# Kernel tuning notes

Hardware: AMD Instinct MI355X
Metric: run time of the kernel (lower is better)

Reference implementation:

```python
import jax, jax.numpy as jnp
import numpy as np


def setup_inputs() -> dict:
    key = jax.random.key(0)
    ks = jax.random.split(key, 18)
    B, L, D, E, V = 64, 4096, 512, 256, 32000
    s = 0.05
    return {
        "featureGrid": jax.random.normal(ks[0], (B, L, D), jnp.float32),
        "y_prev": jax.random.uniform(ks[1], (B, V), jnp.float32),
        "out_prev": jax.random.normal(ks[2], (B, D), jnp.float32),
        "h_prev": jax.random.normal(ks[3], (B, D), jnp.float32),
        "c_prev": jax.random.normal(ks[4], (B, D), jnp.float32),
        "embedding": jax.random.normal(ks[5], (V, E), jnp.float32) * s,
        "W_f": jax.random.normal(ks[6], (D + E, D), jnp.float32) * s,
        "W_i": jax.random.normal(ks[7], (D + E, D), jnp.float32) * s,
        "W_g": jax.random.normal(ks[8], (D + E, D), jnp.float32) * s,
        "W_o": jax.random.normal(ks[9], (D + E, D), jnp.float32) * s,
        "b_f": jax.random.normal(ks[10], (D,), jnp.float32) * s,
        "b_i": jax.random.normal(ks[11], (D,), jnp.float32) * s,
        "b_g": jax.random.normal(ks[12], (D,), jnp.float32) * s,
        "b_o": jax.random.normal(ks[13], (D,), jnp.float32) * s,
        "W_e": jax.random.normal(ks[14], (D, D), jnp.float32) * s,
        "W_out": jax.random.normal(ks[15], (2 * D, D), jnp.float32) * s,
        "W_y": jax.random.normal(ks[16], (D, V), jnp.float32) * s,
    }


def reference(featureGrid, y_prev, out_prev, h_prev, c_prev, embedding,
              W_f, W_i, W_g, W_o, b_f, b_i, b_g, b_o, W_e, W_out, W_y):
    # free_run: previous output distribution -> argmax token -> embedding
    tok = jnp.argmax(y_prev, axis=-1)              # [B]
    emb = embedding[tok]                            # [B, E]
    x = jnp.concatenate([emb, out_prev], axis=-1)   # [B, E+D]
    f = jax.nn.sigmoid(x @ W_f + b_f)
    i = jax.nn.sigmoid(x @ W_i + b_i)
    g = jnp.tanh(x @ W_g + b_g)
    o = jax.nn.sigmoid(x @ W_o + b_o)
    c = c_prev * f + i * g                          # [B, D]
    h = jnp.tanh(c) * o                             # [B, D]
    b = h @ W_e                                     # [B, D]
    e = jnp.einsum('bld,bd->bl', featureGrid, b)    # attention scores [B, L]
    a = jax.nn.softmax(e, axis=-1)                  # [B, L]
    z = jnp.einsum('bl,bld->bd', a, featureGrid)    # context [B, D]
    hz = jnp.concatenate([h, z], axis=-1)           # [B, 2D]
    out = jnp.tanh(hz @ W_out)                      # [B, D]
    y = jax.nn.softmax(out @ W_y, axis=-1)          # [B, V]
    return (y, out, h, c)
```

## Files before the change

kernel.cpp:

```cpp
#include <hip/hip_runtime.h>
#include <math.h>

#define NB 64
#define NL 4096
#define ND 512
#define NE 256
#define NV 32000
#define NX 768
#define CHUNKS 32
#define RPC (NL / CHUNKS)
#define RPW (RPC / 4)
#define NV4 (NV / 4)

#define GK_KS 4
#define GK_KL 192
#define WE_KS 4
#define WE_KL 128
#define WO_KS 4
#define WO_KL 256

typedef float v4f __attribute__((ext_vector_type(4)));
__device__ __forceinline__ float4 ntload4(const float* p) {
    v4f v = __builtin_nontemporal_load((const v4f*)p);
    return make_float4(v[0], v[1], v[2], v[3]);
}

__global__ void k_argmax(const float* __restrict__ y_prev, int* __restrict__ tok) {
    int b = blockIdx.x, tid = threadIdx.x, lane = tid & 63, wave = tid >> 6;
    const float4* row = (const float4*)(y_prev + (size_t)b * NV);
    float best = -INFINITY; int bi = 0x7fffffff;
    for (int v4 = tid; v4 < NV4; v4 += 1024) {
        float4 x = row[v4];
        int base = v4 * 4;
        if (x.x > best) { best = x.x; bi = base; }
        if (x.y > best) { best = x.y; bi = base + 1; }
        if (x.z > best) { best = x.z; bi = base + 2; }
        if (x.w > best) { best = x.w; bi = base + 3; }
    }
    #pragma unroll
    for (int off = 32; off > 0; off >>= 1) {
        float ob = __shfl_xor(best, off, 64);
        int   oi = __shfl_xor(bi, off, 64);
        if (ob > best || (ob == best && oi < bi)) { best = ob; bi = oi; }
    }
    __shared__ float sv[16]; __shared__ int si[16];
    if (lane == 0) { sv[wave] = best; si[wave] = bi; }
    __syncthreads();
    if (tid == 0) {
        float bb = sv[0]; int ii = si[0];
        for (int w = 1; w < 16; ++w)
            if (sv[w] > bb || (sv[w] == bb && si[w] < ii)) { bb = sv[w]; ii = si[w]; }
        tok[b] = ii;
    }
}

__global__ void k_gates(const float* __restrict__ embedding, const float* __restrict__ out_prev,
                        const int* __restrict__ tok,
                        const float* __restrict__ W_f, const float* __restrict__ W_i,
                        const float* __restrict__ W_g, const float* __restrict__ W_o,
                        float* __restrict__ gp) {
    __shared__ float xs[16][GK_KL];
    int tid = threadIdx.x;
    int cc = blockIdx.x, bg = blockIdx.y, ks = blockIdx.z;
    int k0 = ks * GK_KL;
    for (int e = tid; e < 16 * GK_KL; e += 256) {
        int bi = e / GK_KL, kk = e - bi * GK_KL;
        int b = bg * 16 + bi, k = k0 + kk;
        xs[bi][kk] = (k < NE) ? embedding[(size_t)tok[b] * NE + k]
                              : out_prev[(size_t)b * ND + (k - NE)];
    }
    __syncthreads();
    int ct = tid & 63, bs = tid >> 6;
    int gate = cc >> 1;
    int d = (cc & 1) * 256 + ct * 4;
    const float* W = (gate == 0) ? W_f : (gate == 1) ? W_i : (gate == 2) ? W_g : W_o;
    const float4* Wp = (const float4*)(W + (size_t)k0 * ND + d);
    float acc[4][4] = {};
    #pragma unroll 4
    for (int kk = 0; kk < GK_KL; ++kk) {
        float4 w4 = Wp[kk * (ND / 4)];
        #pragma unroll
        for (int i = 0; i < 4; ++i) {
            float xv = xs[bs * 4 + i][kk];
            acc[i][0] += xv * w4.x; acc[i][1] += xv * w4.y;
            acc[i][2] += xv * w4.z; acc[i][3] += xv * w4.w;
        }
    }
    #pragma unroll
    for (int i = 0; i < 4; ++i) {
        int b = bg * 16 + bs * 4 + i;
        float4 st = make_float4(acc[i][0], acc[i][1], acc[i][2], acc[i][3]);
        *(float4*)&gp[(((size_t)ks * 4 + gate) * NB + b) * ND + d] = st;
    }
}

__global__ void k_lstm(const float* __restrict__ gp, const float* __restrict__ c_prev,
                       const float* __restrict__ b_f, const float* __restrict__ b_i,
                       const float* __restrict__ b_g, const float* __restrict__ b_o,
                       float* __restrict__ h_out, float* __restrict__ c_out) {
    int idx = blockIdx.x * 256 + threadIdx.x;
    int b = idx >> 9, d = idx & 511;
    float F = b_f[d], I = b_i[d], G = b_g[d], O = b_o[d];
    #pragma unroll
    for (int ks = 0; ks < GK_KS; ++ks) {
        F += gp[(((size_t)ks * 4 + 0) * NB + b) * ND + d];
        I += gp[(((size_t)ks * 4 + 1) * NB + b) * ND + d];
        G += gp[(((size_t)ks * 4 + 2) * NB + b) * ND + d];
        O += gp[(((size_t)ks * 4 + 3) * NB + b) * ND + d];
    }
    float f = 1.f / (1.f + __expf(-F));
    float i = 1.f / (1.f + __expf(-I));
    float g = tanhf(G);
    float o = 1.f / (1.f + __expf(-O));
    float c = c_prev[idx] * f + i * g;
    float h = tanhf(c) * o;
    h_out[idx] = h;
    c_out[idx] = c;
}

__global__ void k_we(const float* __restrict__ h, const float* __restrict__ W_e,
                     float* __restrict__ wp) {
    __shared__ float hs[16][WE_KL];
    int tid = threadIdx.x;
    int cc = blockIdx.x, bg = blockIdx.y, ks = blockIdx.z;
    int k0 = ks * WE_KL;
    for (int e = tid; e < 16 * WE_KL; e += 256) {
        int bi = e >> 7, kk = e & 127;
        hs[bi][kk] = h[(size_t)(bg * 16 + bi) * ND + k0 + kk];
    }
    __syncthreads();
    int ct = tid & 63, bs = tid >> 6;
    int col = cc * 256 + ct * 4;
    const float4* Wp = (const float4*)(W_e + (size_t)k0 * ND + col);
    float acc[4][4] = {};
    #pragma unroll 4
    for (int kk = 0; kk < WE_KL; ++kk) {
        float4 w4 = Wp[kk * (ND / 4)];
        #pragma unroll
        for (int i = 0; i < 4; ++i) {
            float xv = hs[bs * 4 + i][kk];
            acc[i][0] += xv * w4.x; acc[i][1] += xv * w4.y;
            acc[i][2] += xv * w4.z; acc[i][3] += xv * w4.w;
        }
    }
    #pragma unroll
    for (int i = 0; i < 4; ++i) {
        int b = bg * 16 + bs * 4 + i;
        float4 st = make_float4(acc[i][0], acc[i][1], acc[i][2], acc[i][3]);
        *(float4*)&wp[((size_t)ks * NB + b) * ND + col] = st;
    }
}

__global__ void k_attn(const float* __restrict__ fg, const float* __restrict__ wp,
                       float* __restrict__ partM, float* __restrict__ partS,
                       float* __restrict__ partZ) {
    int blk = blockIdx.x;
    int b = blk / CHUNKS, chunk = blk - b * CHUNKS;
    int tid = threadIdx.x, wave = tid >> 6, lane = tid & 63;
    int lo4 = lane * 4;
    float4 bs0 = make_float4(0.f, 0.f, 0.f, 0.f), bs1 = bs0;
    #pragma unroll
    for (int ks = 0; ks < WE_KS; ++ks) {
        const float* p = wp + ((size_t)ks * NB + b) * ND;
        float4 a = *(const float4*)(p + lo4);
        float4 c = *(const float4*)(p + 256 + lo4);
        bs0.x += a.x; bs0.y += a.y; bs0.z += a.z; bs0.w += a.w;
        bs1.x += c.x; bs1.y += c.y; bs1.z += c.z; bs1.w += c.w;
    }
    const float* rowp = fg + ((size_t)b * NL + (size_t)chunk * RPC + wave * RPW) * ND;
    float m = -INFINITY, s = 0.f;
    float z0 = 0, z1 = 0, z2 = 0, z3 = 0, z4 = 0, z5 = 0, z6 = 0, z7 = 0;
    float4 c0v = ntload4(rowp + lo4);
    float4 c1v = ntload4(rowp + 256 + lo4);
    float4 n0v = ntload4(rowp + ND + lo4);
    float4 n1v = ntload4(rowp + ND + 256 + lo4);
    #pragma unroll 2
    for (int r = 0; r < RPW; ++r) {
        float4 v0 = c0v, v1 = c1v;
        c0v = n0v; c1v = n1v;
        if (r + 2 < RPW) {
            const float* np = rowp + 2 * ND;
            n0v = ntload4(np + lo4);
            n1v = ntload4(np + 256 + lo4);
        }
        float e = v0.x * bs0.x + v0.y * bs0.y + v0.z * bs0.z + v0.w * bs0.w
                + v1.x * bs1.x + v1.y * bs1.y + v1.z * bs1.z + v1.w * bs1.w;
        #pragma unroll
        for (int off = 32; off > 0; off >>= 1) e += __shfl_xor(e, off, 64);
        if (e > m) {
            float sc = __expf(m - e);
            s *= sc;
            z0 *= sc; z1 *= sc; z2 *= sc; z3 *= sc;
            z4 *= sc; z5 *= sc; z6 *= sc; z7 *= sc;
            m = e;
        }
        float w = __expf(e - m);
        s += w;
        z0 += w * v0.x; z1 += w * v0.y; z2 += w * v0.z; z3 += w * v0.w;
        z4 += w * v1.x; z5 += w * v1.y; z6 += w * v1.z; z7 += w * v1.w;
        rowp += ND;
    }
    __shared__ float wm[4], wsum[4], wz[4][ND];
    float* zp = &wz[wave][0];
    zp[lo4 + 0] = z0; zp[lo4 + 1] = z1; zp[lo4 + 2] = z2; zp[lo4 + 3] = z3;
    zp[256 + lo4 + 0] = z4; zp[256 + lo4 + 1] = z5; zp[256 + lo4 + 2] = z6; zp[256 + lo4 + 3] = z7;
    if (lane == 0) { wm[wave] = m; wsum[wave] = s; }
    __syncthreads();
    float M = fmaxf(fmaxf(wm[0], wm[1]), fmaxf(wm[2], wm[3]));
    float e0 = __expf(wm[0] - M), e1 = __expf(wm[1] - M), e2 = __expf(wm[2] - M), e3 = __expf(wm[3] - M);
    if (tid == 0) {
        partM[blk] = M;
        partS[blk] = wsum[0] * e0 + wsum[1] * e1 + wsum[2] * e2 + wsum[3] * e3;
    }
    for (int d = tid; d < ND; d += 256)
        partZ[(size_t)blk * ND + d] = wz[0][d] * e0 + wz[1][d] * e1 + wz[2][d] * e2 + wz[3][d] * e3;
}

__global__ void k_zcomb(const float* __restrict__ partM, const float* __restrict__ partS,
                        const float* __restrict__ partZ, float* __restrict__ z) {
    int b = blockIdx.x, tid = threadIdx.x;
    float M = -INFINITY;
    #pragma unroll
    for (int j = 0; j < CHUNKS; ++j) M = fmaxf(M, partM[b * CHUNKS + j]);
    float w[CHUNKS]; float S = 0.f;
    #pragma unroll
    for (int j = 0; j < CHUNKS; ++j) { w[j] = __expf(partM[b * CHUNKS + j] - M); S += partS[b * CHUNKS + j] * w[j]; }
    float inv = 1.f / S;
    for (int d = tid; d < ND; d += 256) {
        float acc = 0.f;
        #pragma unroll
        for (int j = 0; j < CHUNKS; ++j) acc += w[j] * partZ[((size_t)b * CHUNKS + j) * ND + d];
        z[(size_t)b * ND + d] = acc * inv;
    }
}

__global__ void k_wout(const float* __restrict__ h, const float* __restrict__ z,
                       const float* __restrict__ W_out, float* __restrict__ op) {
    __shared__ float hzs[16][WO_KL];
    int tid = threadIdx.x;
    int cc = blockIdx.x, bg = blockIdx.y, ks = blockIdx.z;
    int k0 = ks * WO_KL;
    for (int e = tid; e < 16 * WO_KL; e += 256) {
        int bi = e >> 8, kk = e & 255;
        int b = bg * 16 + bi, k = k0 + kk;
        hzs[bi][kk] = (k < ND) ? h[(size_t)b * ND + k] : z[(size_t)b * ND + (k - ND)];
    }
    __syncthreads();
    int ct = tid & 63, bs = tid >> 6;
    int col = cc * 256 + ct * 4;
    const float4* Wp = (const float4*)(W_out + (size_t)k0 * ND + col);
    float acc[4][4] = {};
    #pragma unroll 4
    for (int kk = 0; kk < WO_KL; ++kk) {
        float4 w4 = Wp[kk * (ND / 4)];
        #pragma unroll
        for (int i = 0; i < 4; ++i) {
            float xv = hzs[bs * 4 + i][kk];
            acc[i][0] += xv * w4.x; acc[i][1] += xv * w4.y;
            acc[i][2] += xv * w4.z; acc[i][3] += xv * w4.w;
        }
    }
    #pragma unroll
    for (int i = 0; i < 4; ++i) {
        int b = bg * 16 + bs * 4 + i;
        float4 st = make_float4(acc[i][0], acc[i][1], acc[i][2], acc[i][3]);
        *(float4*)&op[((size_t)ks * NB + b) * ND + col] = st;
    }
}

__global__ void k_outfin(const float* __restrict__ op,
                         float* __restrict__ out_f32, float* __restrict__ outT) {
    int idx = blockIdx.x * 512 + threadIdx.x;
    int b = idx >> 9, d = idx & 511;
    float s = 0.f;
    #pragma unroll
    for (int ks = 0; ks < WO_KS; ++ks) s += op[((size_t)ks * NB + b) * ND + d];
    float t = tanhf(s);
    out_f32[idx] = t;
    outT[(size_t)d * NB + b] = t;
}

#define WLOAD(P, G0)                                                          \
    { _Pragma("unroll")                                                       \
      for (int u = 0; u < 8; ++u)                                             \
          P[u] = *(const float4*)(wbase + (size_t)((G0) * 8 + u) * NV); }

#define WCOMP(P, G0)                                                          \
    { _Pragma("unroll")                                                       \
      for (int u = 0; u < 8; ++u) {                                           \
          int dd = ((G0) & 7) * 8 + u;                                        \
          float4 ov = *(const float4*)&os[dd][bq * 4];                        \
          const float ob[4] = {ov.x, ov.y, ov.z, ov.w};                       \
          const float wj[4] = {P[u].x, P[u].y, P[u].z, P[u].w};               \
          _Pragma("unroll")                                                   \
          for (int i = 0; i < 4; ++i) {                                       \
              _Pragma("unroll")                                               \
              for (int j = 0; j < 4; ++j) acc[i][j] += ob[i] * wj[j];         \
          }                                                                   \
      } }

__global__ __launch_bounds__(512, 1) void k_logits(const float* __restrict__ outT,
                                                   const float* __restrict__ W_y,
                                                   float* __restrict__ ylog) {
    __shared__ float os[64][64];
    int tid = threadIdx.x;
    int cg = tid & 31;
    int bq = tid >> 5;
    int c0 = blockIdx.x * 128;
    const float* wbase = W_y + c0 + cg * 4;
    float acc[4][4];
    #pragma unroll
    for (int i = 0; i < 4; ++i)
        #pragma unroll
        for (int j = 0; j < 4; ++j) acc[i][j] = 0.f;
    float4 pA[8], pB[8];
    WLOAD(pA, 0);
    for (int G = 0; G < 64; G += 2) {
        if ((G & 7) == 0) {
            __syncthreads();
            int dt = G >> 3;
            for (int e = tid; e < 4096; e += 512) {
                int dd = e >> 6, bb = e & 63;
                os[dd][bb] = outT[(size_t)(dt * 64 + dd) * NB + bb];
            }
            __syncthreads();
        }
        WLOAD(pB, G + 1);
        WCOMP(pA, G);
        if (G + 2 < 64) WLOAD(pA, G + 2);
        WCOMP(pB, G + 1);
    }
    #pragma unroll
    for (int i = 0; i < 4; ++i) {
        float4 st = make_float4(acc[i][0], acc[i][1], acc[i][2], acc[i][3]);
        *(float4*)&ylog[(size_t)(bq * 4 + i) * NV + c0 + cg * 4] = st;
    }
}

__global__ void k_softmax(float* __restrict__ y) {
    int b = blockIdx.x, tid = threadIdx.x, lane = tid & 63, wave = tid >> 6;
    float4* row = (float4*)(y + (size_t)b * NV);
    float4 r[8];
    int cnt = 0;
    for (int v4 = tid; v4 < NV4; v4 += 1024) r[cnt++] = row[v4];
    float m = -INFINITY;
    for (int k = 0; k < cnt; ++k)
        m = fmaxf(m, fmaxf(fmaxf(r[k].x, r[k].y), fmaxf(r[k].z, r[k].w)));
    #pragma unroll
    for (int off = 32; off > 0; off >>= 1) m = fmaxf(m, __shfl_xor(m, off, 64));
    __shared__ float red[16];
    __shared__ float bcast[2];
    if (lane == 0) red[wave] = m;
    __syncthreads();
    if (tid == 0) {
        float M = red[0];
        for (int w = 1; w < 16; ++w) M = fmaxf(M, red[w]);
        bcast[0] = M;
    }
    __syncthreads();
    float M = bcast[0];
    float s = 0.f;
    for (int k = 0; k < cnt; ++k) {
        r[k].x = __expf(r[k].x - M); r[k].y = __expf(r[k].y - M);
        r[k].z = __expf(r[k].z - M); r[k].w = __expf(r[k].w - M);
        s += r[k].x + r[k].y + r[k].z + r[k].w;
    }
    #pragma unroll
    for (int off = 32; off > 0; off >>= 1) s += __shfl_xor(s, off, 64);
    if (lane == 0) red[wave] = s;
    __syncthreads();
    if (tid == 0) {
        float S = 0.f;
        for (int w = 0; w < 16; ++w) S += red[w];
        bcast[1] = 1.f / S;
    }
    __syncthreads();
    float inv = bcast[1];
    cnt = 0;
    for (int v4 = tid; v4 < NV4; v4 += 1024) {
        float4 e4 = r[cnt++];
        e4.x *= inv; e4.y *= inv; e4.z *= inv; e4.w *= inv;
        row[v4] = e4;
    }
}

extern "C" void kernel_launch(void* const* d_in, const int* in_sizes, int n_in,
                              void* d_out, int out_size, void* d_ws, size_t ws_size,
                              hipStream_t stream) {
    (void)in_sizes; (void)n_in; (void)out_size; (void)ws_size;
    const float* featureGrid = (const float*)d_in[0];
    const float* y_prev      = (const float*)d_in[1];
    const float* out_prev    = (const float*)d_in[2];
    const float* c_prev      = (const float*)d_in[4];
    const float* embedding   = (const float*)d_in[5];
    const float* W_f = (const float*)d_in[6];
    const float* W_i = (const float*)d_in[7];
    const float* W_g = (const float*)d_in[8];
    const float* W_o = (const float*)d_in[9];
    const float* b_f = (const float*)d_in[10];
    const float* b_i = (const float*)d_in[11];
    const float* b_g = (const float*)d_in[12];
    const float* b_o = (const float*)d_in[13];
    const float* W_e   = (const float*)d_in[14];
    const float* W_out = (const float*)d_in[15];
    const float* W_y   = (const float*)d_in[16];

    float* y_f32   = (float*)d_out;
    float* out_f32 = y_f32 + (size_t)NB * NV;
    float* h_f32   = out_f32 + (size_t)NB * ND;
    float* c_f32   = h_f32 + (size_t)NB * ND;

    float* ws = (float*)d_ws;
    int*   tok   = (int*)ws;
    float* gp    = ws + 64;
    float* wp    = gp + (size_t)GK_KS * 4 * NB * ND;
    float* zctx  = wp + (size_t)WE_KS * NB * ND;
    float* partM = zctx + NB * ND;
    float* partS = partM + NB * CHUNKS;
    float* partZ = partS + NB * CHUNKS;
    float* op    = partZ + (size_t)NB * CHUNKS * ND;
    float* outT  = op + (size_t)WO_KS * NB * ND;

    k_argmax<<<NB, 1024, 0, stream>>>(y_prev, tok);
    k_gates<<<dim3(8, 4, GK_KS), 256, 0, stream>>>(embedding, out_prev, tok, W_f, W_i, W_g, W_o, gp);
    k_lstm<<<128, 256, 0, stream>>>(gp, c_prev, b_f, b_i, b_g, b_o, h_f32, c_f32);
    k_we<<<dim3(2, 4, WE_KS), 256, 0, stream>>>(h_f32, W_e, wp);
    k_attn<<<NB * CHUNKS, 256, 0, stream>>>(featureGrid, wp, partM, partS, partZ);
    k_zcomb<<<NB, 256, 0, stream>>>(partM, partS, partZ, zctx);
    k_wout<<<dim3(2, 4, WO_KS), 256, 0, stream>>>(h_f32, zctx, W_out, op);
    k_outfin<<<64, 512, 0, stream>>>(op, out_f32, outT);
    k_logits<<<250, 512, 0, stream>>>(outT, W_y, y_f32);
    k_softmax<<<NB, 1024, 0, stream>>>(y_f32);
}
```

Baseline: 243.9 us.

## Fuse LSTM cell into W_e GEMM and context combine into W_out GEMM

Folds the LSTM elementwise stage into the k_we prologue, so each block recomputes its slice of h and c from the gate partial sums, and only cc==0 blocks write h and c. Folds the attention chunk-combine (k_zcomb) into the k_wout prologue, with each block rebuilding the softmax-weighted context slice from the partial results. The argmax read switches to nontemporal loads. This removes two kernel launches and their global round trips, at the cost of redundant recomputation across blocks and longer serial prologues in small grids.

```diff
diff --git a/kernel.cpp b/kernel.cpp
--- a/kernel.cpp
+++ b/kernel.cpp
@@ -27,10 +27,10 @@
 
 __global__ void k_argmax(const float* __restrict__ y_prev, int* __restrict__ tok) {
     int b = blockIdx.x, tid = threadIdx.x, lane = tid & 63, wave = tid >> 6;
-    const float4* row = (const float4*)(y_prev + (size_t)b * NV);
+    const float* row = y_prev + (size_t)b * NV;
     float best = -INFINITY; int bi = 0x7fffffff;
     for (int v4 = tid; v4 < NV4; v4 += 1024) {
-        float4 x = row[v4];
+        float4 x = ntload4(row + v4 * 4);
         int base = v4 * 4;
         if (x.x > best) { best = x.x; bi = base; }
         if (x.y > best) { best = x.y; bi = base + 1; }
@@ -94,31 +94,11 @@
     }
 }
 
-__global__ void k_lstm(const float* __restrict__ gp, const float* __restrict__ c_prev,
-                       const float* __restrict__ b_f, const float* __restrict__ b_i,
-                       const float* __restrict__ b_g, const float* __restrict__ b_o,
-                       float* __restrict__ h_out, float* __restrict__ c_out) {
-    int idx = blockIdx.x * 256 + threadIdx.x;
-    int b = idx >> 9, d = idx & 511;
-    float F = b_f[d], I = b_i[d], G = b_g[d], O = b_o[d];
-    #pragma unroll
-    for (int ks = 0; ks < GK_KS; ++ks) {
-        F += gp[(((size_t)ks * 4 + 0) * NB + b) * ND + d];
-        I += gp[(((size_t)ks * 4 + 1) * NB + b) * ND + d];
-        G += gp[(((size_t)ks * 4 + 2) * NB + b) * ND + d];
-        O += gp[(((size_t)ks * 4 + 3) * NB + b) * ND + d];
-    }
-    float f = 1.f / (1.f + __expf(-F));
-    float i = 1.f / (1.f + __expf(-I));
-    float g = tanhf(G);
-    float o = 1.f / (1.f + __expf(-O));
-    float c = c_prev[idx] * f + i * g;
-    float h = tanhf(c) * o;
-    h_out[idx] = h;
-    c_out[idx] = c;
-}
-
-__global__ void k_we(const float* __restrict__ h, const float* __restrict__ W_e,
+__global__ void k_we(const float* __restrict__ gp, const float* __restrict__ c_prev,
+                     const float* __restrict__ b_f, const float* __restrict__ b_i,
+                     const float* __restrict__ b_g, const float* __restrict__ b_o,
+                     const float* __restrict__ W_e,
+                     float* __restrict__ h_out, float* __restrict__ c_out,
                      float* __restrict__ wp) {
     __shared__ float hs[16][WE_KL];
     int tid = threadIdx.x;
@@ -126,7 +106,26 @@
     int k0 = ks * WE_KL;
     for (int e = tid; e < 16 * WE_KL; e += 256) {
         int bi = e >> 7, kk = e & 127;
-        hs[bi][kk] = h[(size_t)(bg * 16 + bi) * ND + k0 + kk];
+        int b = bg * 16 + bi, d = k0 + kk;
+        float F = b_f[d], I = b_i[d], G = b_g[d], O = b_o[d];
+        #pragma unroll
+        for (int k2 = 0; k2 < GK_KS; ++k2) {
+            F += gp[(((size_t)k2 * 4 + 0) * NB + b) * ND + d];
+            I += gp[(((size_t)k2 * 4 + 1) * NB + b) * ND + d];
+            G += gp[(((size_t)k2 * 4 + 2) * NB + b) * ND + d];
+            O += gp[(((size_t)k2 * 4 + 3) * NB + b) * ND + d];
+        }
+        float f = 1.f / (1.f + __expf(-F));
+        float i = 1.f / (1.f + __expf(-I));
+        float g = tanhf(G);
+        float o = 1.f / (1.f + __expf(-O));
+        float c = c_prev[(size_t)b * ND + d] * f + i * g;
+        float h = tanhf(c) * o;
+        hs[bi][kk] = h;
+        if (cc == 0) {
+            h_out[(size_t)b * ND + d] = h;
+            c_out[(size_t)b * ND + d] = c;
+        }
     }
     __syncthreads();
     int ct = tid & 63, bs = tid >> 6;
@@ -216,34 +215,45 @@
         partZ[(size_t)blk * ND + d] = wz[0][d] * e0 + wz[1][d] * e1 + wz[2][d] * e2 + wz[3][d] * e3;
 }
 
-__global__ void k_zcomb(const float* __restrict__ partM, const float* __restrict__ partS,
-                        const float* __restrict__ partZ, float* __restrict__ z) {
-    int b = blockIdx.x, tid = threadIdx.x;
-    float M = -INFINITY;
-    #pragma unroll
-    for (int j = 0; j < CHUNKS; ++j) M = fmaxf(M, partM[b * CHUNKS + j]);
-    float w[CHUNKS]; float S = 0.f;
-    #pragma unroll
-    for (int j = 0; j < CHUNKS; ++j) { w[j] = __expf(partM[b * CHUNKS + j] - M); S += partS[b * CHUNKS + j] * w[j]; }
-    float inv = 1.f / S;
-    for (int d = tid; d < ND; d += 256) {
-        float acc = 0.f;
-        #pragma unroll
-        for (int j = 0; j < CHUNKS; ++j) acc += w[j] * partZ[((size_t)b * CHUNKS + j) * ND + d];
-        z[(size_t)b * ND + d] = acc * inv;
-    }
-}
-
-__global__ void k_wout(const float* __restrict__ h, const float* __restrict__ z,
+__global__ void k_wout(const float* __restrict__ h, const float* __restrict__ partM,
+                       const float* __restrict__ partS, const float* __restrict__ partZ,
                        const float* __restrict__ W_out, float* __restrict__ op) {
     __shared__ float hzs[16][WO_KL];
+    __shared__ float wjs[16][CHUNKS];
+    __shared__ float invb[16];
     int tid = threadIdx.x;
     int cc = blockIdx.x, bg = blockIdx.y, ks = blockIdx.z;
     int k0 = ks * WO_KL;
+    if (k0 >= ND && tid < 16) {
+        int b = bg * 16 + tid;
+        float M = -INFINITY;
+        #pragma unroll
+        for (int j = 0; j < CHUNKS; ++j) M = fmaxf(M, partM[b * CHUNKS + j]);
+        float S = 0.f;
+        #pragma unroll
+        for (int j = 0; j < CHUNKS; ++j) {
+            float w = __expf(partM[b * CHUNKS + j] - M);
+            wjs[tid][j] = w;
+            S += partS[b * CHUNKS + j] * w;
+        }
+        invb[tid] = 1.f / S;
+    }
+    __syncthreads();
     for (int e = tid; e < 16 * WO_KL; e += 256) {
         int bi = e >> 8, kk = e & 255;
         int b = bg * 16 + bi, k = k0 + kk;
-        hzs[bi][kk] = (k < ND) ? h[(size_t)b * ND + k] : z[(size_t)b * ND + (k - ND)];
+        float v;
+        if (k < ND) {
+            v = h[(size_t)b * ND + k];
+        } else {
+            int d = k - ND;
+            float acc = 0.f;
+            #pragma unroll
+            for (int j = 0; j < CHUNKS; ++j)
+                acc += wjs[bi][j] * partZ[((size_t)b * CHUNKS + j) * ND + d];
+            v = acc * invb[bi];
+        }
+        hzs[bi][kk] = v;
     }
     __syncthreads();
     int ct = tid & 63, bs = tid >> 6;
@@ -414,8 +424,7 @@
     int*   tok   = (int*)ws;
     float* gp    = ws + 64;
     float* wp    = gp + (size_t)GK_KS * 4 * NB * ND;
-    float* zctx  = wp + (size_t)WE_KS * NB * ND;
-    float* partM = zctx + NB * ND;
+    float* partM = wp + (size_t)WE_KS * NB * ND;
     float* partS = partM + NB * CHUNKS;
     float* partZ = partS + NB * CHUNKS;
     float* op    = partZ + (size_t)NB * CHUNKS * ND;
@@ -423,11 +432,9 @@
 
     k_argmax<<<NB, 1024, 0, stream>>>(y_prev, tok);
     k_gates<<<dim3(8, 4, GK_KS), 256, 0, stream>>>(embedding, out_prev, tok, W_f, W_i, W_g, W_o, gp);
-    k_lstm<<<128, 256, 0, stream>>>(gp, c_prev, b_f, b_i, b_g, b_o, h_f32, c_f32);
-    k_we<<<dim3(2, 4, WE_KS), 256, 0, stream>>>(h_f32, W_e, wp);
+    k_we<<<dim3(2, 4, WE_KS), 256, 0, stream>>>(gp, c_prev, b_f, b_i, b_g, b_o, W_e, h_f32, c_f32, wp);
     k_attn<<<NB * CHUNKS, 256, 0, stream>>>(featureGrid, wp, partM, partS, partZ);
-    k_zcomb<<<NB, 256, 0, stream>>>(partM, partS, partZ, zctx);
-    k_wout<<<dim3(2, 4, WO_KS), 256, 0, stream>>>(h_f32, zctx, W_out, op);
+    k_wout<<<dim3(2, 4, WO_KS), 256, 0, stream>>>(h_f32, partM, partS, partZ, W_out, op);
     k_outfin<<<64, 512, 0, stream>>>(op, out_f32, outT);
     k_logits<<<250, 512, 0, stream>>>(outT, W_y, y_f32);
     k_softmax<<<NB, 1024, 0, stream>>>(y_f32);
```

Result: slower. 255.6 us (+4.8%).
